# Kernel optimization log

Measured on AMD Instinct MI355X. Metric: run time of the kernel, lower is better.

## Reference

```python
import jax, jax.numpy as jnp
import numpy as np

N = 50000      # nodes per graph
E = 1600000    # edges per graph
D_IN = 128
D_HID = 128
D_OUT = 128
D_GF = 128
N_LAYERS = 3   # input->hid, hid->hid (hidden_layer=1), hid->out


def setup_inputs() -> dict:
    key = jax.random.key(0)
    ks = jax.random.split(key, 24)
    inp = {
        "feat_p": jax.random.normal(ks[0], (N, D_IN), jnp.float32),
        "src_p": jax.random.randint(ks[1], (E,), 0, N, jnp.int32),
        "dst_p": jax.random.randint(ks[2], (E,), 0, N, jnp.int32),
        "feat_s": jax.random.normal(ks[3], (N, D_IN), jnp.float32),
        "src_s": jax.random.randint(ks[4], (E,), 0, N, jnp.int32),
        "dst_s": jax.random.randint(ks[5], (E,), 0, N, jnp.int32),
    }
    dims = [(D_IN, D_HID), (D_HID, D_HID), (D_HID, D_OUT)]
    for i, (di, do) in enumerate(dims):
        inp[f"W{i}"] = jax.random.normal(ks[6 + 2 * i], (di, do), jnp.float32) * 0.05
        inp[f"b{i}"] = jnp.zeros((do,), jnp.float32)
    inp["Wr"] = jax.random.normal(ks[14], (D_OUT, D_GF), jnp.float32) * 0.05
    inp["br"] = jnp.zeros((D_GF,), jnp.float32)
    inp["Wm1"] = jax.random.normal(ks[15], (2 * D_GF, D_GF), jnp.float32) * 0.05
    inp["bm1"] = jnp.zeros((D_GF,), jnp.float32)
    inp["Wm2"] = jax.random.normal(ks[16], (D_GF, 1), jnp.float32) * 0.05
    inp["bm2"] = jnp.zeros((1,), jnp.float32)
    return inp


def _gcn_stack(feat, src, dst, layers):
    """Stacked GCN: mean over incoming messages, then linear.
    NOTE: the original SingleGCN never applies its ReLU (bug preserved)."""
    n = feat.shape[0]
    deg = jax.ops.segment_sum(jnp.ones_like(src, feat.dtype), dst, num_segments=n)
    inv_deg = (1.0 / jnp.maximum(deg, 1.0))[:, None]  # [N,1]
    h = feat
    for W, b in layers:
        msg = h[src]                                           # [E,d] gather
        agg = jax.ops.segment_sum(msg, dst, num_segments=n)    # [N,d] scatter-add
        h = (agg * inv_deg) @ W + b                            # mean + linear
    return h


def reference(feat_p, src_p, dst_p, feat_s, src_s, dst_s,
              W0, b0, W1, b1, W2, b2, Wr, br, Wm1, bm1, Wm2, bm2):
    layers = [(W0, b0), (W1, b1), (W2, b2)]
    h_p = _gcn_stack(feat_p, src_p, dst_p, layers)
    h_s = _gcn_stack(feat_s, src_s, dst_s, layers)
    # ReadOut: mean over nodes -> linear -> sigmoid
    g_p = jax.nn.sigmoid(jnp.mean(h_p, axis=0) @ Wr + br)  # [D_GF]
    g_s = jax.nn.sigmoid(jnp.mean(h_s, axis=0) @ Wr + br)
    # Match: concat -> linear -> linear -> sigmoid
    c = jnp.concatenate([g_p, g_s], axis=-1)               # [2*D_GF]
    d = (c @ Wm1 + bm1) @ Wm2 + bm2                        # [1]
    return jax.nn.sigmoid(d)
```

## Files before the change

### kernel.cpp

```cpp
#include <hip/hip_runtime.h>
#include <math.h>

#define D 128
#define BSH 9
#define NPB 512
#define SLOT 128
#define STCAP 6252
#define NBB 256
#define NBKT_MAX 128
#define SB 4
#define CPS (NBB / SB)


__global__ __launch_bounds__(512) void bin_kernel(
        const int* __restrict__ src_p, const int* __restrict__ dst_p,
        const int* __restrict__ src_s, const int* __restrict__ dst_s,
        int* __restrict__ sbins, unsigned short* __restrict__ dbins,
        unsigned* __restrict__ cnt_s, unsigned* __restrict__ cnt_d,
        int E, int nbkt) {
    const int b = blockIdx.x, side = blockIdx.y, g = blockIdx.z;
    const int* src = g ? src_s : src_p;
    const int* dst = g ? dst_s : dst_p;
    const int* key = side ? dst : src;

    __shared__ int stage[STCAP];
    __shared__ unsigned hist[NBKT_MAX], offs[NBKT_MAX], lcur[NBKT_MAX];

    const int tid = threadIdx.x;
    const int wv = tid >> 6, lane = tid & 63;
    for (int i = tid; i < NBKT_MAX; i += 512) hist[i] = 0u;
    __syncthreads();

    const int e0 = b * STCAP;
    const int e1 = min(e0 + STCAP, E);
    const int efull = e0 + ((e1 - e0) & ~3);

    for (int e = e0 + tid * 4; e + 4 <= e1; e += 512 * 4) {
        int4 k4 = *(const int4*)(key + e);
        atomicAdd(&hist[k4.x >> BSH], 1u);
        atomicAdd(&hist[k4.y >> BSH], 1u);
        atomicAdd(&hist[k4.z >> BSH], 1u);
        atomicAdd(&hist[k4.w >> BSH], 1u);
    }
    for (int e = efull + tid; e < e1; e += 512)
        atomicAdd(&hist[key[e] >> BSH], 1u);
    __syncthreads();

    if (wv == 0) {
        unsigned a = (2 * lane < nbkt) ? hist[2 * lane] : 0u;
        unsigned bb = (2 * lane + 1 < nbkt) ? hist[2 * lane + 1] : 0u;
        unsigned v = a + bb;
        for (int d2 = 1; d2 < 64; d2 <<= 1) {
            unsigned t = __shfl_up(v, d2);
            if (lane >= d2) v += t;
        }
        unsigned ex = v - (a + bb);
        if (2 * lane < nbkt) { offs[2 * lane] = ex; lcur[2 * lane] = ex; }
        if (2 * lane + 1 < nbkt) { offs[2 * lane + 1] = ex + a; lcur[2 * lane + 1] = ex + a; }
    }
    __syncthreads();

    if (side == 0) {
        for (int e = e0 + tid * 4; e + 4 <= e1; e += 512 * 4) {
            int4 s4 = *(const int4*)(src + e);
            int4 d4 = *(const int4*)(dst + e);
            int sv[4] = {s4.x, s4.y, s4.z, s4.w};
            int dv[4] = {d4.x, d4.y, d4.z, d4.w};
            #pragma unroll
            for (int k = 0; k < 4; ++k) {
                unsigned p = atomicAdd(&lcur[sv[k] >> BSH], 1u);
                stage[p] = ((sv[k] & (NPB - 1)) << 17) | dv[k];
            }
        }
        for (int e = efull + tid; e < e1; e += 512) {
            int s = src[e], d2 = dst[e];
            unsigned p = atomicAdd(&lcur[s >> BSH], 1u);
            stage[p] = ((s & (NPB - 1)) << 17) | d2;
        }
        __syncthreads();
        int* sb = sbins + (size_t)g * nbkt * NBB * SLOT;
        unsigned* csp = cnt_s + (size_t)g * nbkt * NBB;
        for (int q = wv; q < nbkt; q += 8) {
            unsigned cs = min(hist[q], (unsigned)SLOT);
            unsigned os = offs[q];
            int* dp = sb + ((size_t)q * NBB + b) * SLOT;
            for (unsigned i = lane; i < cs; i += 64) dp[i] = stage[os + i];
            if (lane == 0) csp[q * NBB + b] = cs;
        }
    } else {
        unsigned short* st = (unsigned short*)stage;
        for (int e = e0 + tid * 4; e + 4 <= e1; e += 512 * 4) {
            int4 d4 = *(const int4*)(dst + e);
            int dv[4] = {d4.x, d4.y, d4.z, d4.w};
            #pragma unroll
            for (int k = 0; k < 4; ++k) {
                unsigned p = atomicAdd(&lcur[dv[k] >> BSH], 1u);
                st[p] = (unsigned short)(dv[k] & (NPB - 1));
            }
        }
        for (int e = efull + tid; e < e1; e += 512) {
            int d2 = dst[e];
            unsigned p = atomicAdd(&lcur[d2 >> BSH], 1u);
            st[p] = (unsigned short)(d2 & (NPB - 1));
        }
        __syncthreads();
        unsigned short* db = dbins + (size_t)g * nbkt * NBB * SLOT;
        unsigned* cdp = cnt_d + (size_t)g * nbkt * NBB;
        for (int q = wv; q < nbkt; q += 8) {
            unsigned cd = min(hist[q], (unsigned)SLOT);
            unsigned od = offs[q];
            unsigned short* ddp = db + ((size_t)q * NBB + b) * SLOT;
            for (unsigned i = lane; i < cd; i += 64) ddp[i] = st[od + i];
            if (lane == 0) cdp[q * NBB + b] = cd;
        }
    }
}

__global__ __launch_bounds__(512) void deg_part(
        const unsigned short* __restrict__ dbins, const unsigned* __restrict__ cnt_d,
        float* __restrict__ partials, int nbkt) {
    const int s = blockIdx.x, q = blockIdx.y, g = blockIdx.z;
    const unsigned short* dq = dbins + ((size_t)(g * nbkt + q) * NBB + s * CPS) * SLOT;
    const unsigned* cq = cnt_d + (size_t)(g * nbkt + q) * NBB + s * CPS;
    const int tid = threadIdx.x, wv = tid >> 6;
    __shared__ float bl[8][NPB];
    __shared__ unsigned lcnt[CPS];
    if (tid < CPS) lcnt[tid] = cq[tid];
    for (int i = tid; i < 8 * NPB; i += 512) ((float*)bl)[i] = 0.f;
    __syncthreads();
    float* mybl = bl[wv];
    const ushort4* d4 = (const ushort4*)dq;
    ushort4 v[4]; int limv[4];
    #pragma unroll
    for (int it = 0; it < 4; ++it) {
        int i = it * 512 + tid;
        int lim = (int)lcnt[i >> 5] - ((i & 31) << 2);
        limv[it] = lim;
        if (lim > 0) v[it] = d4[i];
    }
    #pragma unroll
    for (int it = 0; it < 4; ++it) {
        if (limv[it] <= 0) continue;
        atomicAdd(&mybl[v[it].x], 1.f);
        if (limv[it] > 1) atomicAdd(&mybl[v[it].y], 1.f);
        if (limv[it] > 2) atomicAdd(&mybl[v[it].z], 1.f);
        if (limv[it] > 3) atomicAdd(&mybl[v[it].w], 1.f);
    }
    __syncthreads();
    float* pp = partials + (((size_t)(g * nbkt + q)) * SB + s) * NPB;
    for (int i = tid; i < NPB; i += 512) {
        float t = 0.f;
        #pragma unroll
        for (int r = 0; r < 8; ++r) t += bl[r][i];
        pp[i] = t;
    }
}

__global__ __launch_bounds__(512) void deg_combine(
        const float* __restrict__ partials, float* __restrict__ inv,
        float* __restrict__ zbase, int zcount, int N, int nbkt) {
    const int q = blockIdx.x, g = blockIdx.y;
    const int tid = threadIdx.x;
    if (q == 0 && g == 0)
        for (int i = tid; i < zcount; i += 512) zbase[i] = 0.f;
    const float* pp = partials + ((size_t)(g * nbkt + q)) * SB * NPB;
    float t = 0.f;
    #pragma unroll
    for (int s = 0; s < SB; ++s) t += pp[s * NPB + tid];
    const int node = q * NPB + tid;
    if (node < N) inv[(size_t)g * N + node] = 1.0f / fmaxf(t, 1.0f);
}

__global__ __launch_bounds__(512) void part_scan(
        const int* __restrict__ sbins, const unsigned* __restrict__ cnt_s,
        const float* __restrict__ w, float* __restrict__ partials,
        int N, int nbkt) {
    const int s = blockIdx.x, q = blockIdx.y, g = blockIdx.z;
    const int* sq = sbins + ((size_t)(g * nbkt + q) * NBB + s * CPS) * SLOT;
    const unsigned* cq = cnt_s + (size_t)(g * nbkt + q) * NBB + s * CPS;
    const float* wg = w + (size_t)g * N;
    const int tid = threadIdx.x, wv = tid >> 6;
    __shared__ float bl[8][NPB];
    __shared__ unsigned lcnt[CPS];
    if (tid < CPS) lcnt[tid] = cq[tid];
    for (int i = tid; i < 8 * NPB; i += 512) ((float*)bl)[i] = 0.f;
    __syncthreads();
    float* mybl = bl[wv];
    const int4* s4 = (const int4*)sq;
    int4 v[4]; int limv[4];
    #pragma unroll
    for (int it = 0; it < 4; ++it) {
        int i = it * 512 + tid;
        int lim = (int)lcnt[i >> 5] - ((i & 31) << 2);
        limv[it] = lim;
        if (lim > 0) v[it] = s4[i];
    }
    float va[4][4];
    #pragma unroll
    for (int it = 0; it < 4; ++it) {
        if (limv[it] <= 0) continue;
        va[it][0] = wg[v[it].x & 0x1FFFF];
        va[it][1] = (limv[it] > 1) ? wg[v[it].y & 0x1FFFF] : 0.f;
        va[it][2] = (limv[it] > 2) ? wg[v[it].z & 0x1FFFF] : 0.f;
        va[it][3] = (limv[it] > 3) ? wg[v[it].w & 0x1FFFF] : 0.f;
    }
    #pragma unroll
    for (int it = 0; it < 4; ++it) {
        if (limv[it] <= 0) continue;
        atomicAdd(&mybl[((unsigned)v[it].x) >> 17], va[it][0]);
        if (limv[it] > 1) atomicAdd(&mybl[((unsigned)v[it].y) >> 17], va[it][1]);
        if (limv[it] > 2) atomicAdd(&mybl[((unsigned)v[it].z) >> 17], va[it][2]);
        if (limv[it] > 3) atomicAdd(&mybl[((unsigned)v[it].w) >> 17], va[it][3]);
    }
    __syncthreads();
    float* pp = partials + (((size_t)(g * nbkt + q)) * SB + s) * NPB;
    for (int i = tid; i < NPB; i += 512) {
        float t = 0.f;
        #pragma unroll
        for (int r = 0; r < 8; ++r) t += bl[r][i];
        pp[i] = t;
    }
}

__global__ __launch_bounds__(512) void prop_combine(
        const float* __restrict__ partials, const float* __restrict__ inv,
        float* __restrict__ out_w, float* __restrict__ sums, int s_idx,
        int N, int nbkt, float scale) {
    const int q = blockIdx.x, g = blockIdx.y;
    const int tid = threadIdx.x;
    const float* pp = partials + ((size_t)(g * nbkt + q)) * SB * NPB;
    float t = 0.f;
    #pragma unroll
    for (int s = 0; s < SB; ++s) t += pp[s * NPB + tid];
    const float u = t * scale;
    const int node = q * NPB + tid;
    const bool valid = node < N;
    if (valid) {
        size_t off = (size_t)g * N + node;
        out_w[off] = u * inv[off];
    }
    __shared__ float red[NPB];
    red[tid] = valid ? u : 0.f;
    __syncthreads();
    for (int st = 256; st > 0; st >>= 1) {
        if (tid < st) red[tid] += red[tid + st];
        __syncthreads();
    }
    if (tid == 0 && red[0] != 0.f) atomicAdd(&sums[g * 2 + s_idx], red[0]);
}

__global__ __launch_bounds__(512) void feat_combine(
        const float* __restrict__ partials,
        const float* __restrict__ feat_p, const float* __restrict__ feat_s,
        float* __restrict__ fpart2, int N, int nbkt) {
    const int r = blockIdx.x, q = blockIdx.y, g = blockIdx.z;
    const int tid = threadIdx.x;
    const int base = q * NPB + r * 64;
    __shared__ float tmp[4][64];
    __shared__ float red[64];
    __shared__ float4 sm4[512];
    const float* pp = partials + ((size_t)(g * nbkt + q)) * SB * NPB + r * 64;
    if (tid < 256) {
        int s = tid >> 6, n = tid & 63;
        tmp[s][n] = pp[(size_t)s * NPB + n];
    }
    __syncthreads();
    if (tid < 64) {
        float t = tmp[0][tid] + tmp[1][tid] + tmp[2][tid] + tmp[3][tid];
        red[tid] = (base + tid < N) ? t : 0.f;
    }
    __syncthreads();
    const float* feat = g ? feat_s : feat_p;
    const float4* f4 = (const float4*)feat;
    const int col4 = tid & 31, rg = tid >> 5;
    float4 acc = make_float4(0.f, 0.f, 0.f, 0.f);
    #pragma unroll
    for (int k = 0; k < 4; ++k) {
        int row = rg * 4 + k;
        if (base + row < N) {
            float uu = red[row];
            float4 fv = f4[(size_t)(base + row) * 32 + col4];
            acc.x += uu * fv.x; acc.y += uu * fv.y;
            acc.z += uu * fv.z; acc.w += uu * fv.w;
        }
    }
    sm4[tid] = acc;
    __syncthreads();
    for (int st = 8; st > 0; st >>= 1) {
        if (rg < st) {
            float4 o = sm4[(rg + st) * 32 + col4];
            float4 a = sm4[rg * 32 + col4];
            a.x += o.x; a.y += o.y; a.z += o.z; a.w += o.w;
            sm4[rg * 32 + col4] = a;
        }
        __syncthreads();
    }
    if (tid < 32) {
        float4 t = sm4[tid];
        float* dstp = fpart2 + ((size_t)g * 32 + ((q * 8 + r) & 31)) * D + tid * 4;
        atomicAdd(dstp + 0, t.x);
        atomicAdd(dstp + 1, t.y);
        atomicAdd(dstp + 2, t.z);
        atomicAdd(dstp + 3, t.w);
    }
}

__global__ __launch_bounds__(1024) void final_kernel(
        const float* __restrict__ fpart2,
        const float* __restrict__ sums,
        const float* __restrict__ W0, const float* __restrict__ b0,
        const float* __restrict__ W1, const float* __restrict__ b1,
        const float* __restrict__ W2, const float* __restrict__ b2,
        const float* __restrict__ Wr, const float* __restrict__ br,
        const float* __restrict__ Wm1, const float* __restrict__ bm1,
        const float* __restrict__ Wm2, const float* __restrict__ bm2,
        float* __restrict__ out) {
    __shared__ float x[2][128];
    __shared__ float part[2][4][128];
    __shared__ float rvec[256];
    __shared__ float Avec[128], Bvec[128];
    __shared__ float gv[256];
    __shared__ float m1[128];
    const int tid = threadIdx.x;
    const int j = tid & 127;
    const int h = (tid >> 7) & 3;
    const int gg = tid >> 9;

    auto mv128 = [&](const float* __restrict__ W, float* __restrict__ buf) {
        float p = 0.f;
        const float* Wp = W + (size_t)(h * 32) * 128 + j;
        #pragma unroll
        for (int i = 0; i < 32; ++i) p += buf[h * 32 + i] * Wp[(size_t)i * 128];
        part[gg][h][j] = p;
        __syncthreads();
        if (h == 0)
            buf[j] = part[gg][0][j] + part[gg][1][j] + part[gg][2][j] + part[gg][3][j];
        __syncthreads();
    };

    if (tid < 256) {
        int g = tid >> 7;
        const float* fp = fpart2 + (size_t)g * 4096 + (tid & 127);
        float rv = 0.f;
        #pragma unroll
        for (int b = 0; b < 32; ++b) rv += fp[(size_t)b * 128];
        rvec[tid] = rv;
    }
    __syncthreads();

    if (h == 0) x[gg][j] = b0[j];
    __syncthreads();
    mv128(W1, x[gg]);
    mv128(W2, x[gg]);
    if (tid < 128) Avec[j] = x[0][j];
    __syncthreads();
    if (h == 0) x[gg][j] = b1[j];
    __syncthreads();
    mv128(W2, x[gg]);
    if (tid < 128) Bvec[j] = x[0][j];
    __syncthreads();

    {
        const float s1 = sums[gg * 2 + 0];
        const float s2 = sums[gg * 2 + 1];
        if (h == 0) x[gg][j] = rvec[gg * 128 + j];
        __syncthreads();
        mv128(W0, x[gg]);
        mv128(W1, x[gg]);
        mv128(W2, x[gg]);
        if (h == 0) x[gg][j] += s2 * Avec[j] + s1 * Bvec[j] + b2[j];
        __syncthreads();
        mv128(Wr, x[gg]);
        if (h == 0) gv[gg * 128 + j] = 1.0f / (1.0f + expf(-(x[gg][j] + br[j])));
        __syncthreads();
    }

    {
        float p = 0.f;
        const float* Wp = Wm1 + (size_t)(h * 64) * 128 + j;
        #pragma unroll
        for (int i = 0; i < 64; ++i) p += gv[h * 64 + i] * Wp[(size_t)i * 128];
        part[gg][h][j] = p;
        __syncthreads();
        if (tid < 128)
            m1[j] = (part[0][0][j] + part[0][1][j] + part[0][2][j] + part[0][3][j]
                     + bm1[j]) * Wm2[j];
        __syncthreads();
        if (tid < 64) m1[tid] += m1[tid + 64];
        __syncthreads();
        if (tid < 32) m1[tid] += m1[tid + 32];
        __syncthreads();
        if (tid < 16) m1[tid] += m1[tid + 16];
        __syncthreads();
        if (tid < 8) m1[tid] += m1[tid + 8];
        __syncthreads();
        if (tid < 4) m1[tid] += m1[tid + 4];
        __syncthreads();
        if (tid < 2) m1[tid] += m1[tid + 2];
        __syncthreads();
        if (tid == 0) out[0] = 1.0f / (1.0f + expf(-(m1[0] + m1[1] + bm2[0])));
    }
}

extern "C" void kernel_launch(void* const* d_in, const int* in_sizes, int n_in,
                              void* d_out, int out_size, void* d_ws, size_t ws_size,
                              hipStream_t stream) {
    const float* feat_p = (const float*)d_in[0];
    const int*   src_p  = (const int*)d_in[1];
    const int*   dst_p  = (const int*)d_in[2];
    const float* feat_s = (const float*)d_in[3];
    const int*   src_s  = (const int*)d_in[4];
    const int*   dst_s  = (const int*)d_in[5];
    const float* W0 = (const float*)d_in[6];
    const float* b0 = (const float*)d_in[7];
    const float* W1 = (const float*)d_in[8];
    const float* b1 = (const float*)d_in[9];
    const float* W2 = (const float*)d_in[10];
    const float* b2 = (const float*)d_in[11];
    const float* Wr = (const float*)d_in[12];
    const float* br = (const float*)d_in[13];
    const float* Wm1 = (const float*)d_in[14];
    const float* bm1 = (const float*)d_in[15];
    const float* Wm2 = (const float*)d_in[16];
    const float* bm2 = (const float*)d_in[17];
    float* out = (float*)d_out;

    const int N = in_sizes[0] / D;
    const int E = in_sizes[1];
    const int N2 = 2 * N;
    const int nbkt = (N + NPB - 1) >> BSH;

    float* ws     = (float*)d_ws;
    float* sums   = ws;
    float* fpart2 = ws + 16;
    float* inv    = fpart2 + 2 * 32 * 128;
    float* w1     = inv + N2;
    float* w2     = w1 + N2;
    float* partials = w2 + N2;
    unsigned* cnt_s = (unsigned*)(partials + (size_t)2 * nbkt * SB * NPB);
    unsigned* cnt_d = cnt_s + (size_t)2 * nbkt * NBB;
    int* sbins    = (int*)(cnt_d + (size_t)2 * nbkt * NBB);
    unsigned short* dbins = (unsigned short*)(sbins + (size_t)2 * nbkt * NBB * SLOT);

    const float u0 = 1.0f / (float)N;
    const int zcount = 16 + 2 * 32 * 128;

    bin_kernel<<<dim3(NBB, 2, 2), 512, 0, stream>>>(src_p, dst_p, src_s, dst_s,
                                                    sbins, dbins, cnt_s, cnt_d,
                                                    E, nbkt);

    deg_part<<<dim3(SB, nbkt, 2), 512, 0, stream>>>(dbins, cnt_d, partials, nbkt);
    deg_combine<<<dim3(nbkt, 2), 512, 0, stream>>>(partials, inv, ws, zcount,
                                                   N, nbkt);

    part_scan<<<dim3(SB, nbkt, 2), 512, 0, stream>>>(sbins, cnt_s, inv,
                                                     partials, N, nbkt);
    prop_combine<<<dim3(nbkt, 2), 512, 0, stream>>>(partials, inv, w1,
                                                    sums, 0, N, nbkt, u0);

    part_scan<<<dim3(SB, nbkt, 2), 512, 0, stream>>>(sbins, cnt_s, w1,
                                                     partials, N, nbkt);
    prop_combine<<<dim3(nbkt, 2), 512, 0, stream>>>(partials, inv, w2,
                                                    sums, 1, N, nbkt, 1.0f);

    part_scan<<<dim3(SB, nbkt, 2), 512, 0, stream>>>(sbins, cnt_s, w2,
                                                     partials, N, nbkt);
    feat_combine<<<dim3(8, nbkt, 2), 512, 0, stream>>>(partials, feat_p, feat_s,
                                                       fpart2, N, nbkt);

    final_kernel<<<1, 1024, 0, stream>>>(fpart2, sums, W0, b0, W1, b1, W2, b2,
                                         Wr, br, Wm1, bm1, Wm2, bm2, out);
}
```

Measured before the change: 292.6 us.

## Split edge scans into smaller blocks, precompute W1·W2, use shuffle reductions

SB doubles to 8, so deg_part and part_scan now run twice as many 256-thread blocks, each with four smaller shared histograms, and edge loads become unconditional with masked indices. A new wprep kernel precomputes W1·W2 and the bias-propagation vectors off the serial final kernel's critical path. prop_combine swaps its shared-memory tree reduction for wavefront shuffles, and feat_combine now sums over SB partials. Unconditional loads may read stale bin slots, which are masked and discarded. The extra launch and larger partials buffer add overhead.

```diff
diff --git a/kernel.cpp b/kernel.cpp
--- a/kernel.cpp
+++ b/kernel.cpp
@@ -8,7 +8,7 @@
 #define STCAP 6252
 #define NBB 256
 #define NBKT_MAX 128
-#define SB 4
+#define SB 8
 #define CPS (NBB / SB)
 
 
@@ -116,44 +116,39 @@
     }
 }
 
-__global__ __launch_bounds__(512) void deg_part(
+__global__ __launch_bounds__(256) void deg_part(
         const unsigned short* __restrict__ dbins, const unsigned* __restrict__ cnt_d,
         float* __restrict__ partials, int nbkt) {
     const int s = blockIdx.x, q = blockIdx.y, g = blockIdx.z;
     const unsigned short* dq = dbins + ((size_t)(g * nbkt + q) * NBB + s * CPS) * SLOT;
     const unsigned* cq = cnt_d + (size_t)(g * nbkt + q) * NBB + s * CPS;
     const int tid = threadIdx.x, wv = tid >> 6;
-    __shared__ float bl[8][NPB];
+    __shared__ float bl[4][NPB];
     __shared__ unsigned lcnt[CPS];
     if (tid < CPS) lcnt[tid] = cq[tid];
-    for (int i = tid; i < 8 * NPB; i += 512) ((float*)bl)[i] = 0.f;
+    for (int i = tid; i < 4 * NPB; i += 256) ((float*)bl)[i] = 0.f;
     __syncthreads();
     float* mybl = bl[wv];
     const ushort4* d4 = (const ushort4*)dq;
     ushort4 v[4]; int limv[4];
     #pragma unroll
+    for (int it = 0; it < 4; ++it) v[it] = d4[it * 256 + tid];
+    #pragma unroll
     for (int it = 0; it < 4; ++it) {
-        int i = it * 512 + tid;
-        int lim = (int)lcnt[i >> 5] - ((i & 31) << 2);
-        limv[it] = lim;
-        if (lim > 0) v[it] = d4[i];
+        int i = it * 256 + tid;
+        limv[it] = (int)lcnt[i >> 5] - ((i & 31) << 2);
     }
     #pragma unroll
     for (int it = 0; it < 4; ++it) {
-        if (limv[it] <= 0) continue;
-        atomicAdd(&mybl[v[it].x], 1.f);
-        if (limv[it] > 1) atomicAdd(&mybl[v[it].y], 1.f);
-        if (limv[it] > 2) atomicAdd(&mybl[v[it].z], 1.f);
-        if (limv[it] > 3) atomicAdd(&mybl[v[it].w], 1.f);
+        if (limv[it] > 0) atomicAdd(&mybl[v[it].x & 511], 1.f);
+        if (limv[it] > 1) atomicAdd(&mybl[v[it].y & 511], 1.f);
+        if (limv[it] > 2) atomicAdd(&mybl[v[it].z & 511], 1.f);
+        if (limv[it] > 3) atomicAdd(&mybl[v[it].w & 511], 1.f);
     }
     __syncthreads();
     float* pp = partials + (((size_t)(g * nbkt + q)) * SB + s) * NPB;
-    for (int i = tid; i < NPB; i += 512) {
-        float t = 0.f;
-        #pragma unroll
-        for (int r = 0; r < 8; ++r) t += bl[r][i];
-        pp[i] = t;
-    }
+    for (int i = tid; i < NPB; i += 256)
+        pp[i] = bl[0][i] + bl[1][i] + bl[2][i] + bl[3][i];
 }
 
 __global__ __launch_bounds__(512) void deg_combine(
@@ -171,7 +166,7 @@
     if (node < N) inv[(size_t)g * N + node] = 1.0f / fmaxf(t, 1.0f);
 }
 
-__global__ __launch_bounds__(512) void part_scan(
+__global__ __launch_bounds__(256) void part_scan(
         const int* __restrict__ sbins, const unsigned* __restrict__ cnt_s,
         const float* __restrict__ w, float* __restrict__ partials,
         int N, int nbkt) {
@@ -180,46 +175,40 @@
     const unsigned* cq = cnt_s + (size_t)(g * nbkt + q) * NBB + s * CPS;
     const float* wg = w + (size_t)g * N;
     const int tid = threadIdx.x, wv = tid >> 6;
-    __shared__ float bl[8][NPB];
+    __shared__ float bl[4][NPB];
     __shared__ unsigned lcnt[CPS];
     if (tid < CPS) lcnt[tid] = cq[tid];
-    for (int i = tid; i < 8 * NPB; i += 512) ((float*)bl)[i] = 0.f;
+    for (int i = tid; i < 4 * NPB; i += 256) ((float*)bl)[i] = 0.f;
     __syncthreads();
     float* mybl = bl[wv];
     const int4* s4 = (const int4*)sq;
     int4 v[4]; int limv[4];
     #pragma unroll
+    for (int it = 0; it < 4; ++it) v[it] = s4[it * 256 + tid];
+    #pragma unroll
     for (int it = 0; it < 4; ++it) {
-        int i = it * 512 + tid;
-        int lim = (int)lcnt[i >> 5] - ((i & 31) << 2);
-        limv[it] = lim;
-        if (lim > 0) v[it] = s4[i];
+        int i = it * 256 + tid;
+        limv[it] = (int)lcnt[i >> 5] - ((i & 31) << 2);
     }
     float va[4][4];
     #pragma unroll
     for (int it = 0; it < 4; ++it) {
-        if (limv[it] <= 0) continue;
         va[it][0] = wg[v[it].x & 0x1FFFF];
-        va[it][1] = (limv[it] > 1) ? wg[v[it].y & 0x1FFFF] : 0.f;
-        va[it][2] = (limv[it] > 2) ? wg[v[it].z & 0x1FFFF] : 0.f;
-        va[it][3] = (limv[it] > 3) ? wg[v[it].w & 0x1FFFF] : 0.f;
+        va[it][1] = wg[v[it].y & 0x1FFFF];
+        va[it][2] = wg[v[it].z & 0x1FFFF];
+        va[it][3] = wg[v[it].w & 0x1FFFF];
     }
     #pragma unroll
     for (int it = 0; it < 4; ++it) {
-        if (limv[it] <= 0) continue;
-        atomicAdd(&mybl[((unsigned)v[it].x) >> 17], va[it][0]);
-        if (limv[it] > 1) atomicAdd(&mybl[((unsigned)v[it].y) >> 17], va[it][1]);
-        if (limv[it] > 2) atomicAdd(&mybl[((unsigned)v[it].z) >> 17], va[it][2]);
-        if (limv[it] > 3) atomicAdd(&mybl[((unsigned)v[it].w) >> 17], va[it][3]);
+        if (limv[it] > 0) atomicAdd(&mybl[(((unsigned)v[it].x) >> 17) & 511], va[it][0]);
+        if (limv[it] > 1) atomicAdd(&mybl[(((unsigned)v[it].y) >> 17) & 511], va[it][1]);
+        if (limv[it] > 2) atomicAdd(&mybl[(((unsigned)v[it].z) >> 17) & 511], va[it][2]);
+        if (limv[it] > 3) atomicAdd(&mybl[(((unsigned)v[it].w) >> 17) & 511], va[it][3]);
     }
     __syncthreads();
     float* pp = partials + (((size_t)(g * nbkt + q)) * SB + s) * NPB;
-    for (int i = tid; i < NPB; i += 512) {
-        float t = 0.f;
-        #pragma unroll
-        for (int r = 0; r < 8; ++r) t += bl[r][i];
-        pp[i] = t;
-    }
+    for (int i = tid; i < NPB; i += 256)
+        pp[i] = bl[0][i] + bl[1][i] + bl[2][i] + bl[3][i];
 }
 
 __global__ __launch_bounds__(512) void prop_combine(
@@ -227,7 +216,7 @@
         float* __restrict__ out_w, float* __restrict__ sums, int s_idx,
         int N, int nbkt, float scale) {
     const int q = blockIdx.x, g = blockIdx.y;
-    const int tid = threadIdx.x;
+    const int tid = threadIdx.x, wv = tid >> 6, lane = tid & 63;
     const float* pp = partials + ((size_t)(g * nbkt + q)) * SB * NPB;
     float t = 0.f;
     #pragma unroll
@@ -239,14 +228,17 @@
         size_t off = (size_t)g * N + node;
         out_w[off] = u * inv[off];
     }
-    __shared__ float red[NPB];
-    red[tid] = valid ? u : 0.f;
-    __syncthreads();
-    for (int st = 256; st > 0; st >>= 1) {
-        if (tid < st) red[tid] += red[tid + st];
-        __syncthreads();
-    }
-    if (tid == 0 && red[0] != 0.f) atomicAdd(&sums[g * 2 + s_idx], red[0]);
+    float r = valid ? u : 0.f;
+    #pragma unroll
+    for (int off = 32; off > 0; off >>= 1) r += __shfl_down(r, off);
+    __shared__ float wsum[8];
+    if (lane == 0) wsum[wv] = r;
+    __syncthreads();
+    if (tid == 0) {
+        float s = wsum[0] + wsum[1] + wsum[2] + wsum[3]
+                + wsum[4] + wsum[5] + wsum[6] + wsum[7];
+        if (s != 0.f) atomicAdd(&sums[g * 2 + s_idx], s);
+    }
 }
 
 __global__ __launch_bounds__(512) void feat_combine(
@@ -256,17 +248,19 @@
     const int r = blockIdx.x, q = blockIdx.y, g = blockIdx.z;
     const int tid = threadIdx.x;
     const int base = q * NPB + r * 64;
-    __shared__ float tmp[4][64];
+    __shared__ float tmp[SB][64];
     __shared__ float red[64];
     __shared__ float4 sm4[512];
     const float* pp = partials + ((size_t)(g * nbkt + q)) * SB * NPB + r * 64;
-    if (tid < 256) {
+    {
         int s = tid >> 6, n = tid & 63;
         tmp[s][n] = pp[(size_t)s * NPB + n];
     }
     __syncthreads();
     if (tid < 64) {
-        float t = tmp[0][tid] + tmp[1][tid] + tmp[2][tid] + tmp[3][tid];
+        float t = 0.f;
+        #pragma unroll
+        for (int s = 0; s < SB; ++s) t += tmp[s][tid];
         red[tid] = (base + tid < N) ? t : 0.f;
     }
     __syncthreads();
@@ -305,12 +299,48 @@
     }
 }
 
+__global__ __launch_bounds__(256) void wprep(
+        const float* __restrict__ W1, const float* __restrict__ W2,
+        const float* __restrict__ b0, const float* __restrict__ b1,
+        float* __restrict__ T0, float* __restrict__ Av, float* __restrict__ Bv) {
+    const int b = blockIdx.x, tid = threadIdx.x;
+    if (b < 64) {
+        const int row = 2 * b + (tid >> 7), col = tid & 127;
+        float acc = 0.f;
+        const float* w1r = W1 + (size_t)row * 128;
+        #pragma unroll 8
+        for (int k = 0; k < 128; ++k) acc += w1r[k] * W2[(size_t)k * 128 + col];
+        T0[(size_t)row * 128 + col] = acc;
+    } else if (b == 64) {
+        __shared__ float bv[128];
+        if (tid < 128) {
+            float a = 0.f;
+            #pragma unroll 8
+            for (int i = 0; i < 128; ++i) a += b0[i] * W1[(size_t)i * 128 + tid];
+            bv[tid] = a;
+        }
+        __syncthreads();
+        if (tid < 128) {
+            float a = 0.f;
+            #pragma unroll 8
+            for (int i = 0; i < 128; ++i) a += bv[i] * W2[(size_t)i * 128 + tid];
+            Av[tid] = a;
+        }
+    } else {
+        if (tid < 128) {
+            float a = 0.f;
+            #pragma unroll 8
+            for (int i = 0; i < 128; ++i) a += b1[i] * W2[(size_t)i * 128 + tid];
+            Bv[tid] = a;
+        }
+    }
+}
+
 __global__ __launch_bounds__(1024) void final_kernel(
-        const float* __restrict__ fpart2,
-        const float* __restrict__ sums,
-        const float* __restrict__ W0, const float* __restrict__ b0,
-        const float* __restrict__ W1, const float* __restrict__ b1,
-        const float* __restrict__ W2, const float* __restrict__ b2,
+        const float* __restrict__ fpart2, const float* __restrict__ sums,
+        const float* __restrict__ W0, const float* __restrict__ T0,
+        const float* __restrict__ Av, const float* __restrict__ Bv,
+        const float* __restrict__ b2,
         const float* __restrict__ Wr, const float* __restrict__ br,
         const float* __restrict__ Wm1, const float* __restrict__ bm1,
         const float* __restrict__ Wm2, const float* __restrict__ bm2,
@@ -318,7 +348,6 @@
     __shared__ float x[2][128];
     __shared__ float part[2][4][128];
     __shared__ float rvec[256];
-    __shared__ float Avec[128], Bvec[128];
     __shared__ float gv[256];
     __shared__ float m1[128];
     const int tid = threadIdx.x;
@@ -348,27 +377,14 @@
     }
     __syncthreads();
 
-    if (h == 0) x[gg][j] = b0[j];
-    __syncthreads();
-    mv128(W1, x[gg]);
-    mv128(W2, x[gg]);
-    if (tid < 128) Avec[j] = x[0][j];
-    __syncthreads();
-    if (h == 0) x[gg][j] = b1[j];
-    __syncthreads();
-    mv128(W2, x[gg]);
-    if (tid < 128) Bvec[j] = x[0][j];
-    __syncthreads();
-
     {
         const float s1 = sums[gg * 2 + 0];
         const float s2 = sums[gg * 2 + 1];
         if (h == 0) x[gg][j] = rvec[gg * 128 + j];
         __syncthreads();
         mv128(W0, x[gg]);
-        mv128(W1, x[gg]);
-        mv128(W2, x[gg]);
-        if (h == 0) x[gg][j] += s2 * Avec[j] + s1 * Bvec[j] + b2[j];
+        mv128(T0, x[gg]);
+        if (h == 0) x[gg][j] += s2 * Av[j] + s1 * Bv[j] + b2[j];
         __syncthreads();
         mv128(Wr, x[gg]);
         if (h == 0) gv[gg * 128 + j] = 1.0f / (1.0f + expf(-(x[gg][j] + br[j])));
@@ -433,7 +449,10 @@
     float* ws     = (float*)d_ws;
     float* sums   = ws;
     float* fpart2 = ws + 16;
-    float* inv    = fpart2 + 2 * 32 * 128;
+    float* T0     = fpart2 + 2 * 32 * 128;
+    float* Av     = T0 + 128 * 128;
+    float* Bv     = Av + 128;
+    float* inv    = Bv + 128;
     float* w1     = inv + N2;
     float* w2     = w1 + N2;
     float* partials = w2 + N2;
@@ -445,29 +464,31 @@
     const float u0 = 1.0f / (float)N;
     const int zcount = 16 + 2 * 32 * 128;
 
+    wprep<<<66, 256, 0, stream>>>(W1, W2, b0, b1, T0, Av, Bv);
+
     bin_kernel<<<dim3(NBB, 2, 2), 512, 0, stream>>>(src_p, dst_p, src_s, dst_s,
                                                     sbins, dbins, cnt_s, cnt_d,
                                                     E, nbkt);
 
-    deg_part<<<dim3(SB, nbkt, 2), 512, 0, stream>>>(dbins, cnt_d, partials, nbkt);
+    deg_part<<<dim3(SB, nbkt, 2), 256, 0, stream>>>(dbins, cnt_d, partials, nbkt);
     deg_combine<<<dim3(nbkt, 2), 512, 0, stream>>>(partials, inv, ws, zcount,
                                                    N, nbkt);
 
-    part_scan<<<dim3(SB, nbkt, 2), 512, 0, stream>>>(sbins, cnt_s, inv,
+    part_scan<<<dim3(SB, nbkt, 2), 256, 0, stream>>>(sbins, cnt_s, inv,
                                                      partials, N, nbkt);
     prop_combine<<<dim3(nbkt, 2), 512, 0, stream>>>(partials, inv, w1,
                                                     sums, 0, N, nbkt, u0);
 
-    part_scan<<<dim3(SB, nbkt, 2), 512, 0, stream>>>(sbins, cnt_s, w1,
+    part_scan<<<dim3(SB, nbkt, 2), 256, 0, stream>>>(sbins, cnt_s, w1,
                                                      partials, N, nbkt);
     prop_combine<<<dim3(nbkt, 2), 512, 0, stream>>>(partials, inv, w2,
                                                     sums, 1, N, nbkt, 1.0f);
 
-    part_scan<<<dim3(SB, nbkt, 2), 512, 0, stream>>>(sbins, cnt_s, w2,
+    part_scan<<<dim3(SB, nbkt, 2), 256, 0, stream>>>(sbins, cnt_s, w2,
                                                      partials, N, nbkt);
     feat_combine<<<dim3(8, nbkt, 2), 512, 0, stream>>>(partials, feat_p, feat_s,
                                                        fpart2, N, nbkt);
 
-    final_kernel<<<1, 1024, 0, stream>>>(fpart2, sums, W0, b0, W1, b1, W2, b2,
+    final_kernel<<<1, 1024, 0, stream>>>(fpart2, sums, W0, T0, Av, Bv, b2,
                                          Wr, br, Wm1, bm1, Wm2, bm2, out);
 }
```

Result: faster. 275.4 us (-5.9%).
